# Kernel optimization log

Hardware: AMD Instinct MI355X
Metric: run time of the kernel (lower is better)

## Reference

```python
import jax, jax.numpy as jnp
import numpy as np

D_MODEL = 512
D_FF = 2048
N_EXPERTS = 8


def setup_inputs() -> dict:
    key = jax.random.key(0)
    ks = jax.random.split(key, 7)
    scale_in = 1.0 / np.sqrt(D_MODEL)
    scale_ff = 1.0 / np.sqrt(D_FF)
    x = jax.random.normal(ks[0], (4, 2048, D_MODEL), dtype=jnp.float32)
    w1 = jax.random.uniform(ks[1], (N_EXPERTS, D_MODEL, D_FF), jnp.float32, -scale_in, scale_in)
    b1 = jax.random.uniform(ks[2], (N_EXPERTS, D_FF), jnp.float32, -scale_in, scale_in)
    w2 = jax.random.uniform(ks[3], (N_EXPERTS, D_FF, D_MODEL), jnp.float32, -scale_ff, scale_ff)
    b2 = jax.random.uniform(ks[4], (N_EXPERTS, D_MODEL), jnp.float32, -scale_ff, scale_ff)
    wr = jax.random.uniform(ks[5], (D_MODEL, N_EXPERTS), jnp.float32, -scale_in, scale_in)
    br = jax.random.uniform(ks[6], (N_EXPERTS,), jnp.float32, -scale_in, scale_in)
    return {"x": x, "w1": w1, "b1": b1, "w2": w2, "b2": b2, "wr": wr, "br": br}


def reference(x, w1, b1, w2, b2, wr, br):
    # router softmax over experts: [b, t, e]
    route_weights = jax.nn.softmax(x @ wr + br, axis=-1)
    # all-experts FFN: h: [e, b, t, f]
    h = jax.nn.gelu(jnp.einsum('btd,edf->ebtf', x, w1) + b1[:, None, None, :],
                    approximate=False)
    # expert outputs weighted-summed: [b, t, d]
    expert_out = jnp.einsum('ebtf,efd->ebtd', h, w2) + b2[:, None, None, :]
    final_output = jnp.einsum('ebtd,bte->btd', expert_out, route_weights)
    return final_output, route_weights
```

## Files before the change

### kernel.cpp

```cpp
#include <hip/hip_runtime.h>
#include <math.h>

#define D_MODEL 512
#define D_FF    2048
#define N_EXP   8
#define N_TOK   8192
#define BM      64
#define BF      64

typedef _Float16 half8 __attribute__((ext_vector_type(8)));
typedef float    f32x4 __attribute__((ext_vector_type(4)));

__device__ __forceinline__ void gload_lds16(const void* g, void* lds) {
  __builtin_amdgcn_global_load_lds(
      (const __attribute__((address_space(1))) unsigned int*)g,
      (__attribute__((address_space(3))) unsigned int*)lds, 16, 0, 0);
}

__global__ void cvt_x_kernel(const float* __restrict__ x, _Float16* __restrict__ xb) {
  int i = blockIdx.x * blockDim.x + threadIdx.x;
  const float4* xp = (const float4*)x + (size_t)i * 2;
  float4 v0 = xp[0], v1 = xp[1];
  half8 o;
  o[0] = (_Float16)v0.x; o[1] = (_Float16)v0.y; o[2] = (_Float16)v0.z; o[3] = (_Float16)v0.w;
  o[4] = (_Float16)v1.x; o[5] = (_Float16)v1.y; o[6] = (_Float16)v1.z; o[7] = (_Float16)v1.w;
  ((half8*)xb)[i] = o;
}

__global__ void transpose_cvt_kernel(const float* __restrict__ in, _Float16* __restrict__ out,
                                     int R, int C) {
  __shared__ float t[32][33];
  int e = blockIdx.z, rb = blockIdx.y, cb = blockIdx.x;
  int tx = threadIdx.x & 31, ty = threadIdx.x >> 5;
  const float* src = in + ((size_t)e * R + rb * 32) * C + cb * 32;
#pragma unroll
  for (int i = 0; i < 32; i += 8) t[ty + i][tx] = src[(size_t)(ty + i) * C + tx];
  __syncthreads();
  _Float16* dst = out + ((size_t)e * C + cb * 32) * R + rb * 32;
#pragma unroll
  for (int i = 0; i < 32; i += 8) dst[(size_t)(ty + i) * R + tx] = (_Float16)t[tx][ty + i];
}

__global__ void router_kernel(const float* __restrict__ x, const float* __restrict__ wr,
                              const float* __restrict__ br, float* __restrict__ route) {
  int t = (blockIdx.x * blockDim.x + threadIdx.x) >> 6;
  int lane = threadIdx.x & 63;
  const float4* xp = (const float4*)(x + (size_t)t * D_MODEL) + lane * 2;
  float4 xv0 = xp[0], xv1 = xp[1];
  float xv[8] = {xv0.x, xv0.y, xv0.z, xv0.w, xv1.x, xv1.y, xv1.z, xv1.w};
  float acc[8] = {0, 0, 0, 0, 0, 0, 0, 0};
  int d0 = lane * 8;
#pragma unroll
  for (int i = 0; i < 8; ++i) {
    const float4* wp = (const float4*)(wr + (size_t)(d0 + i) * N_EXP);
    float4 w0 = wp[0], w1v = wp[1];
    acc[0] += xv[i] * w0.x;  acc[1] += xv[i] * w0.y;
    acc[2] += xv[i] * w0.z;  acc[3] += xv[i] * w0.w;
    acc[4] += xv[i] * w1v.x; acc[5] += xv[i] * w1v.y;
    acc[6] += xv[i] * w1v.z; acc[7] += xv[i] * w1v.w;
  }
#pragma unroll
  for (int off = 32; off > 0; off >>= 1)
#pragma unroll
    for (int e2 = 0; e2 < 8; ++e2) acc[e2] += __shfl_xor(acc[e2], off);
  float mx = -1e30f;
#pragma unroll
  for (int e2 = 0; e2 < 8; ++e2) { acc[e2] += br[e2]; mx = fmaxf(mx, acc[e2]); }
  float s = 0.f;
#pragma unroll
  for (int e2 = 0; e2 < 8; ++e2) { acc[e2] = expf(acc[e2] - mx); s += acc[e2]; }
  float inv = 1.f / s;
  if (lane < 8) route[(size_t)t * N_EXP + lane] = acc[lane] * inv;
}

__device__ __forceinline__ void stage_A_half(const _Float16* __restrict__ w1t, int e, int f0,
                                             int khalf, char* dst, int w, int l, int i0) {
#pragma unroll
  for (int i = i0; i < i0 + 2; ++i) {
    const int n  = i * 8 + w;
    const int f  = 2 * n + (l >> 5);
    const int sp = (l & 31) ^ (f & 31);
    gload_lds16(w1t + ((size_t)e * D_FF + f0 + f) * D_MODEL + khalf * 256 + sp * 8,
                dst + n * 1024);
  }
}
__device__ __forceinline__ void stage_B_half(const _Float16* __restrict__ w2t, int e, int f0,
                                             int dh, char* dst, int w, int l, int i0) {
#pragma unroll
  for (int i = i0; i < i0 + 2; ++i) {
    const int n  = i * 8 + w;
    const int d  = 8 * n + (l >> 3);
    const int sp = (l & 7) ^ (d & 7);
    gload_lds16(w2t + ((size_t)e * D_MODEL + dh * 256 + d) * D_FF + f0 + sp * 8,
                dst + n * 1024);
  }
}

__global__ __launch_bounds__(512, 2)
void moe_main_kernel(const _Float16* __restrict__ xb, const _Float16* __restrict__ w1t,
                     const _Float16* __restrict__ w2t, const float* __restrict__ b1,
                     const float* __restrict__ b2, const float* __restrict__ route,
                     float* __restrict__ out) {
  __shared__ __align__(16) unsigned char chA[2][32768];
  __shared__ __align__(16) unsigned char chB[2][32768];
  __shared__ __align__(16) unsigned char hs[BM * 128];
  __shared__ _Float16 b1_lds[4 * D_FF];
  __shared__ float routes_lds[4][BM];

  const int tid = threadIdx.x;
  const int l   = tid & 63;
  const int w   = tid >> 6;
  const int eb  = 4 * blockIdx.y;
  const int m0  = blockIdx.x * BM;

  const int mq  = w & 3;
  const int fh  = w >> 2;
  const int mh2 = w & 1;
  const int dq4 = w >> 1;

#pragma unroll
  for (int i = 0; i < 16; ++i) {
    int idx = i * 512 + tid;
    b1_lds[idx] = (_Float16)b1[(size_t)(eb + (idx >> 11)) * D_FF + (idx & 2047)];
  }
  if (tid < 4 * BM)
    routes_lds[tid >> 6][tid & 63] = route[(size_t)(m0 + (tid & 63)) * N_EXP + eb + (tid >> 6)];
  asm volatile("s_waitcnt lgkmcnt(0)" ::: "memory");

  half8 xfrag[16];
  {
    const _Float16* xrow = xb + (size_t)(m0 + 16 * mq + (l & 15)) * D_MODEL + (l >> 4) * 8;
#pragma unroll
    for (int ks = 0; ks < 16; ++ks)
      xfrag[ks] = *(const half8*)(xrow + ks * 32);
  }

  f32x4 acc[2][8];
#pragma unroll
  for (int a = 0; a < 2; ++a)
#pragma unroll
    for (int b = 0; b < 8; ++b) acc[a][b] = (f32x4){0.f, 0.f, 0.f, 0.f};

  stage_A_half(w1t, eb, 0, 0, (char*)chA[0], w, l, 0);
  stage_A_half(w1t, eb, 0, 0, (char*)chA[0], w, l, 2);
  stage_A_half(w1t, eb, 0, 1, (char*)chA[1], w, l, 0);
  stage_A_half(w1t, eb, 0, 1, (char*)chA[1], w, l, 2);
  stage_B_half(w2t, eb, 0, 0, (char*)chB[0], w, l, 0);
  stage_B_half(w2t, eb, 0, 0, (char*)chB[0], w, l, 2);
  asm volatile("s_waitcnt vmcnt(8)" ::: "memory");
  __builtin_amdgcn_s_barrier();

#pragma unroll 1
  for (int ei = 0; ei < 4; ++ei) {
    const int e = eb + ei;
#pragma unroll 1
    for (int fc = 0; fc < 32; ++fc) {
      const int f0 = fc * BF;
      int f0N = f0 + BF, eN = e;
      if (f0N == D_FF) { f0N = 0; eN = (ei < 3) ? e + 1 : eb; }

      float b1v[2];
#pragma unroll
      for (int j = 0; j < 2; ++j)
        b1v[j] = (float)b1_lds[ei * D_FF + f0 + 32 * fh + 16 * j + (l & 15)];

      f32x4 hacc[2];
      hacc[0] = (f32x4){0.f, 0.f, 0.f, 0.f};
      hacc[1] = (f32x4){0.f, 0.f, 0.f, 0.f};

#pragma unroll
      for (int kq = 0; kq < 4; ++kq) {
        const unsigned char* cA = chA[kq >> 1];
        const int q = kq & 1;
        half8 bfr[4][2];
#pragma unroll
        for (int t = 0; t < 4; ++t)
#pragma unroll
          for (int j = 0; j < 2; ++j) {
            const int f  = 32 * fh + 16 * j + (l & 15);
            const int g  = q * 16 + t * 4 + (l >> 4);
            const int sw = (g ^ f) & 31;
            bfr[t][j] = *(const half8*)(cA + f * 512 + sw * 16);
          }
        if      (kq == 0) stage_B_half(w2t, e,  f0,  1, (char*)chB[1], w, l, 0);
        else if (kq == 1) stage_B_half(w2t, e,  f0,  1, (char*)chB[1], w, l, 2);
        else if (kq == 2) stage_A_half(w1t, eN, f0N, 0, (char*)chA[0], w, l, 0);
        else              stage_A_half(w1t, eN, f0N, 0, (char*)chA[0], w, l, 2);
        if (kq & 1) asm volatile("s_waitcnt vmcnt(8)" ::: "memory");
        __builtin_amdgcn_s_barrier();
        asm volatile("s_waitcnt lgkmcnt(0)" ::: "memory");
        __builtin_amdgcn_s_setprio(1);
#pragma unroll
        for (int t = 0; t < 4; ++t) {
          hacc[0] = __builtin_amdgcn_mfma_f32_16x16x32_f16(xfrag[kq * 4 + t], bfr[t][0], hacc[0], 0, 0, 0);
          hacc[1] = __builtin_amdgcn_mfma_f32_16x16x32_f16(xfrag[kq * 4 + t], bfr[t][1], hacc[1], 0, 0, 0);
        }
        __builtin_amdgcn_s_setprio(0);
        if (kq == 3) {
#pragma unroll
          for (int j = 0; j < 2; ++j) {
#pragma unroll
            for (int r = 0; r < 4; ++r) {
              const int m      = 16 * mq + (l >> 4) * 4 + r;
              const int flocal = 32 * fh + 16 * j + (l & 15);
              float v  = hacc[j][r] + b1v[j];
              float u  = v * (1.5957691f + 0.0713548f * v * v);
              float E  = __expf(u);
              float gl = v * E / (E + 1.0f);
              gl *= routes_lds[ei][m];
              const int sh = (flocal >> 3) ^ ((m ^ (m >> 1)) & 7);
              *(_Float16*)(hs + m * 128 + sh * 16 + (flocal & 7) * 2) = (_Float16)gl;
            }
          }
          asm volatile("s_waitcnt lgkmcnt(0)" ::: "memory");
        }
        __builtin_amdgcn_s_barrier();
      }

      half8 a2c[2][2];
#pragma unroll
      for (int c = 0; c < 4; ++c) {
        const int h  = c >> 1;
        const int kh = c & 1;
        if (h == 0) {
#pragma unroll
          for (int mi2 = 0; mi2 < 2; ++mi2) {
            const int mr = 32 * mh2 + 16 * mi2 + (l & 15);
            const int sh = (kh * 4 + (l >> 4)) ^ ((mr ^ (mr >> 1)) & 7);
            a2c[kh][mi2] = *(const half8*)(hs + mr * 128 + sh * 16);
          }
        }
        half8 b2f[4];
#pragma unroll
        for (int jn = 0; jn < 4; ++jn) {
          const int row = dq4 * 64 + jn * 16 + (l & 15);
          const int sw  = (kh * 4 + (l >> 4)) ^ (row & 7);
          b2f[jn] = *(const half8*)(chB[h] + row * 128 + sw * 16);
        }
        if      (c == 0) stage_A_half(w1t, eN, f0N, 1, (char*)chA[1], w, l, 0);
        else if (c == 1) stage_A_half(w1t, eN, f0N, 1, (char*)chA[1], w, l, 2);
        else if (c == 2) stage_B_half(w2t, eN, f0N, 0, (char*)chB[0], w, l, 0);
        else             stage_B_half(w2t, eN, f0N, 0, (char*)chB[0], w, l, 2);
        if (c & 1) asm volatile("s_waitcnt vmcnt(8)" ::: "memory");
        __builtin_amdgcn_s_barrier();
        asm volatile("s_waitcnt lgkmcnt(0)" ::: "memory");
        __builtin_amdgcn_s_setprio(1);
#pragma unroll
        for (int jn = 0; jn < 4; ++jn) {
          acc[0][h * 4 + jn] = __builtin_amdgcn_mfma_f32_16x16x32_f16(a2c[kh][0], b2f[jn], acc[0][h * 4 + jn], 0, 0, 0);
          acc[1][h * 4 + jn] = __builtin_amdgcn_mfma_f32_16x16x32_f16(a2c[kh][1], b2f[jn], acc[1][h * 4 + jn], 0, 0, 0);
        }
        __builtin_amdgcn_s_setprio(0);
        __builtin_amdgcn_s_barrier();
      }
    }
  }

  asm volatile("s_waitcnt vmcnt(0)" ::: "memory");

#pragma unroll
  for (int h = 0; h < 2; ++h)
#pragma unroll
    for (int jn = 0; jn < 4; ++jn) {
      const int dcol = h * 256 + dq4 * 64 + jn * 16 + (l & 15);
      float b2v[4];
#pragma unroll
      for (int ei = 0; ei < 4; ++ei) b2v[ei] = b2[(size_t)(eb + ei) * D_MODEL + dcol];
#pragma unroll
      for (int mi2 = 0; mi2 < 2; ++mi2)
#pragma unroll
        for (int r = 0; r < 4; ++r) {
          const int m = 32 * mh2 + 16 * mi2 + (l >> 4) * 4 + r;
          float add = 0.f;
#pragma unroll
          for (int ei = 0; ei < 4; ++ei) add += routes_lds[ei][m] * b2v[ei];
          unsafeAtomicAdd(out + (size_t)(m0 + m) * D_MODEL + dcol, acc[mi2][h * 4 + jn][r] + add);
        }
    }
}

extern "C" void kernel_launch(void* const* d_in, const int* in_sizes, int n_in,
                              void* d_out, int out_size, void* d_ws, size_t ws_size,
                              hipStream_t stream) {
  (void)in_sizes; (void)n_in; (void)out_size; (void)ws_size;
  const float* x  = (const float*)d_in[0];
  const float* w1 = (const float*)d_in[1];
  const float* b1 = (const float*)d_in[2];
  const float* w2 = (const float*)d_in[3];
  const float* b2 = (const float*)d_in[4];
  const float* wr = (const float*)d_in[5];
  const float* br = (const float*)d_in[6];
  float* out   = (float*)d_out;
  float* route = out + (size_t)N_TOK * D_MODEL;

  char* ws = (char*)d_ws;
  _Float16* xb  = (_Float16*)ws;
  _Float16* w1t = (_Float16*)(ws + (size_t)N_TOK * D_MODEL * 2);
  _Float16* w2t = (_Float16*)(ws + (size_t)N_TOK * D_MODEL * 2
                                 + (size_t)N_EXP * D_FF * D_MODEL * 2);

  hipMemsetAsync(out, 0, (size_t)N_TOK * D_MODEL * sizeof(float), stream);
  cvt_x_kernel<<<(N_TOK * D_MODEL / 8) / 256, 256, 0, stream>>>(x, xb);
  transpose_cvt_kernel<<<dim3(D_FF / 32, D_MODEL / 32, N_EXP), 256, 0, stream>>>(w1, w1t, D_MODEL, D_FF);
  transpose_cvt_kernel<<<dim3(D_MODEL / 32, D_FF / 32, N_EXP), 256, 0, stream>>>(w2, w2t, D_FF, D_MODEL);
  router_kernel<<<N_TOK / 4, 256, 0, stream>>>(x, wr, br, route);
  moe_main_kernel<<<dim3(N_TOK / BM, 2), 512, 0, stream>>>(xb, w1t, w2t, b1, b2, route, out);
}
```

Baseline: 457.9 us.

## Split GEMM1 K-dimension across wave groups and cut per-step barriers

Changes the first GEMM's work split: instead of each wave owning a 16-row M slice over the full K, waves now own 32x32 output tiles over half of K. The two partial sums are reduced through the shared-memory h buffer before GELU. Prefetch staging and barriers are reorganized so far fewer s_barrier calls run per F chunk. The goal is to lower synchronization overhead and halve the per-wave x fragment registers. The cost is an extra LDS round trip for the reduction, and the hand-tuned vmcnt waits carry a correctness risk if they are wrong.

Result: slower. 615.2 us (+34.3%).

```diff
diff --git a/kernel.cpp b/kernel.cpp
--- a/kernel.cpp
+++ b/kernel.cpp
@@ -113,8 +113,9 @@
   const int eb  = 4 * blockIdx.y;
   const int m0  = blockIdx.x * BM;
 
-  const int mq  = w & 3;
-  const int fh  = w >> 2;
+  const int mh1 = w & 1;
+  const int fh1 = (w >> 1) & 1;
+  const int khg = w >> 2;
   const int mh2 = w & 1;
   const int dq4 = w >> 1;
 
@@ -127,12 +128,14 @@
     routes_lds[tid >> 6][tid & 63] = route[(size_t)(m0 + (tid & 63)) * N_EXP + eb + (tid >> 6)];
   asm volatile("s_waitcnt lgkmcnt(0)" ::: "memory");
 
-  half8 xfrag[16];
-  {
-    const _Float16* xrow = xb + (size_t)(m0 + 16 * mq + (l & 15)) * D_MODEL + (l >> 4) * 8;
-#pragma unroll
-    for (int ks = 0; ks < 16; ++ks)
-      xfrag[ks] = *(const half8*)(xrow + ks * 32);
+  half8 xfrag[2][8];
+#pragma unroll
+  for (int mi = 0; mi < 2; ++mi) {
+    const _Float16* xrow = xb + (size_t)(m0 + 32 * mh1 + 16 * mi + (l & 15)) * D_MODEL
+                              + khg * 256 + (l >> 4) * 8;
+#pragma unroll
+    for (int ks = 0; ks < 8; ++ks)
+      xfrag[mi][ks] = *(const half8*)(xrow + ks * 32);
   }
 
   f32x4 acc[2][8];
@@ -147,7 +150,6 @@
   stage_A_half(w1t, eb, 0, 1, (char*)chA[1], w, l, 2);
   stage_B_half(w2t, eb, 0, 0, (char*)chB[0], w, l, 0);
   stage_B_half(w2t, eb, 0, 0, (char*)chB[0], w, l, 2);
-  asm volatile("s_waitcnt vmcnt(8)" ::: "memory");
   __builtin_amdgcn_s_barrier();
 
 #pragma unroll 1
@@ -159,69 +161,102 @@
       int f0N = f0 + BF, eN = e;
       if (f0N == D_FF) { f0N = 0; eN = (ei < 3) ? e + 1 : eb; }
 
-      float b1v[2];
-#pragma unroll
-      for (int j = 0; j < 2; ++j)
-        b1v[j] = (float)b1_lds[ei * D_FF + f0 + 32 * fh + 16 * j + (l & 15)];
-
-      f32x4 hacc[2];
-      hacc[0] = (f32x4){0.f, 0.f, 0.f, 0.f};
-      hacc[1] = (f32x4){0.f, 0.f, 0.f, 0.f};
-
-#pragma unroll
-      for (int kq = 0; kq < 4; ++kq) {
-        const unsigned char* cA = chA[kq >> 1];
-        const int q = kq & 1;
-        half8 bfr[4][2];
-#pragma unroll
-        for (int t = 0; t < 4; ++t)
+      f32x4 hacc[2][2];
+#pragma unroll
+      for (int mi = 0; mi < 2; ++mi)
+#pragma unroll
+        for (int j = 0; j < 2; ++j) hacc[mi][j] = (f32x4){0.f, 0.f, 0.f, 0.f};
+
+#pragma unroll
+      for (int p = 0; p < 4; ++p) {
+        if (p == 0) {
+          stage_B_half(w2t, e, f0, 1, (char*)chB[1], w, l, 0);
+          asm volatile("s_waitcnt vmcnt(6)" ::: "memory");
+          __builtin_amdgcn_s_barrier();
+        } else if (p == 1) {
+          stage_B_half(w2t, e, f0, 1, (char*)chB[1], w, l, 2);
+        }
+        half8 bfr[2][2];
+#pragma unroll
+        for (int ks2 = 0; ks2 < 2; ++ks2)
 #pragma unroll
           for (int j = 0; j < 2; ++j) {
-            const int f  = 32 * fh + 16 * j + (l & 15);
-            const int g  = q * 16 + t * 4 + (l >> 4);
+            const int f  = 32 * fh1 + 16 * j + (l & 15);
+            const int g  = (p * 2 + ks2) * 4 + (l >> 4);
             const int sw = (g ^ f) & 31;
-            bfr[t][j] = *(const half8*)(cA + f * 512 + sw * 16);
+            bfr[ks2][j] = *(const half8*)(chA[khg] + f * 512 + sw * 16);
           }
-        if      (kq == 0) stage_B_half(w2t, e,  f0,  1, (char*)chB[1], w, l, 0);
-        else if (kq == 1) stage_B_half(w2t, e,  f0,  1, (char*)chB[1], w, l, 2);
-        else if (kq == 2) stage_A_half(w1t, eN, f0N, 0, (char*)chA[0], w, l, 0);
-        else              stage_A_half(w1t, eN, f0N, 0, (char*)chA[0], w, l, 2);
-        if (kq & 1) asm volatile("s_waitcnt vmcnt(8)" ::: "memory");
-        __builtin_amdgcn_s_barrier();
         asm volatile("s_waitcnt lgkmcnt(0)" ::: "memory");
         __builtin_amdgcn_s_setprio(1);
 #pragma unroll
-        for (int t = 0; t < 4; ++t) {
-          hacc[0] = __builtin_amdgcn_mfma_f32_16x16x32_f16(xfrag[kq * 4 + t], bfr[t][0], hacc[0], 0, 0, 0);
-          hacc[1] = __builtin_amdgcn_mfma_f32_16x16x32_f16(xfrag[kq * 4 + t], bfr[t][1], hacc[1], 0, 0, 0);
-        }
+        for (int ks2 = 0; ks2 < 2; ++ks2)
+#pragma unroll
+          for (int j = 0; j < 2; ++j) {
+            hacc[0][j] = __builtin_amdgcn_mfma_f32_16x16x32_f16(xfrag[0][p * 2 + ks2], bfr[ks2][j], hacc[0][j], 0, 0, 0);
+            hacc[1][j] = __builtin_amdgcn_mfma_f32_16x16x32_f16(xfrag[1][p * 2 + ks2], bfr[ks2][j], hacc[1][j], 0, 0, 0);
+          }
         __builtin_amdgcn_s_setprio(0);
-        if (kq == 3) {
-#pragma unroll
-          for (int j = 0; j < 2; ++j) {
+      }
+
+      if (khg == 0) {
+#pragma unroll
+        for (int mi = 0; mi < 2; ++mi)
+#pragma unroll
+          for (int j = 0; j < 2; ++j)
 #pragma unroll
             for (int r = 0; r < 4; ++r) {
-              const int m      = 16 * mq + (l >> 4) * 4 + r;
-              const int flocal = 32 * fh + 16 * j + (l & 15);
-              float v  = hacc[j][r] + b1v[j];
+              const int m  = 32 * mh1 + 16 * mi + (l >> 4) * 4 + r;
+              const int fl = 32 * fh1 + 16 * j + (l & 15);
+              const int sh = (fl >> 3) ^ ((m ^ (m >> 1)) & 7);
+              *(_Float16*)(hs + m * 128 + sh * 16 + (fl & 7) * 2) = (_Float16)hacc[mi][j][r];
+            }
+        asm volatile("s_waitcnt lgkmcnt(0)" ::: "memory");
+      }
+      __builtin_amdgcn_s_barrier();
+      if (khg == 1) {
+        float b1v[2];
+#pragma unroll
+        for (int j = 0; j < 2; ++j)
+          b1v[j] = (float)b1_lds[ei * D_FF + f0 + 32 * fh1 + 16 * j + (l & 15)];
+#pragma unroll
+        for (int mi = 0; mi < 2; ++mi)
+#pragma unroll
+          for (int j = 0; j < 2; ++j)
+#pragma unroll
+            for (int r = 0; r < 4; ++r) {
+              const int m  = 32 * mh1 + 16 * mi + (l >> 4) * 4 + r;
+              const int fl = 32 * fh1 + 16 * j + (l & 15);
+              const int sh = (fl >> 3) ^ ((m ^ (m >> 1)) & 7);
+              _Float16* ptr = (_Float16*)(hs + m * 128 + sh * 16 + (fl & 7) * 2);
+              float v  = (float)*ptr + hacc[mi][j][r] + b1v[j];
               float u  = v * (1.5957691f + 0.0713548f * v * v);
               float E  = __expf(u);
               float gl = v * E / (E + 1.0f);
               gl *= routes_lds[ei][m];
-              const int sh = (flocal >> 3) ^ ((m ^ (m >> 1)) & 7);
-              *(_Float16*)(hs + m * 128 + sh * 16 + (flocal & 7) * 2) = (_Float16)gl;
+              *ptr = (_Float16)gl;
             }
-          }
-          asm volatile("s_waitcnt lgkmcnt(0)" ::: "memory");
-        }
-        __builtin_amdgcn_s_barrier();
+        asm volatile("s_waitcnt lgkmcnt(0)" ::: "memory");
       }
+      asm volatile("s_waitcnt vmcnt(4)" ::: "memory");
+      __builtin_amdgcn_s_barrier();
 
       half8 a2c[2][2];
 #pragma unroll
       for (int c = 0; c < 4; ++c) {
         const int h  = c >> 1;
         const int kh = c & 1;
+        if (c == 0) {
+          stage_A_half(w1t, eN, f0N, 0, (char*)chA[0], w, l, 0);
+          stage_A_half(w1t, eN, f0N, 0, (char*)chA[0], w, l, 2);
+        } else if (c == 1) {
+          stage_A_half(w1t, eN, f0N, 1, (char*)chA[1], w, l, 0);
+          stage_A_half(w1t, eN, f0N, 1, (char*)chA[1], w, l, 2);
+          asm volatile("s_waitcnt vmcnt(8)" ::: "memory");
+          __builtin_amdgcn_s_barrier();
+        } else if (c == 2) {
+          stage_B_half(w2t, eN, f0N, 0, (char*)chB[0], w, l, 0);
+          stage_B_half(w2t, eN, f0N, 0, (char*)chB[0], w, l, 2);
+        }
         if (h == 0) {
 #pragma unroll
           for (int mi2 = 0; mi2 < 2; ++mi2) {
@@ -237,12 +272,6 @@
           const int sw  = (kh * 4 + (l >> 4)) ^ (row & 7);
           b2f[jn] = *(const half8*)(chB[h] + row * 128 + sw * 16);
         }
-        if      (c == 0) stage_A_half(w1t, eN, f0N, 1, (char*)chA[1], w, l, 0);
-        else if (c == 1) stage_A_half(w1t, eN, f0N, 1, (char*)chA[1], w, l, 2);
-        else if (c == 2) stage_B_half(w2t, eN, f0N, 0, (char*)chB[0], w, l, 0);
-        else             stage_B_half(w2t, eN, f0N, 0, (char*)chB[0], w, l, 2);
-        if (c & 1) asm volatile("s_waitcnt vmcnt(8)" ::: "memory");
-        __builtin_amdgcn_s_barrier();
         asm volatile("s_waitcnt lgkmcnt(0)" ::: "memory");
         __builtin_amdgcn_s_setprio(1);
 #pragma unroll
@@ -251,7 +280,6 @@
           acc[1][h * 4 + jn] = __builtin_amdgcn_mfma_f32_16x16x32_f16(a2c[kh][1], b2f[jn], acc[1][h * 4 + jn], 0, 0, 0);
         }
         __builtin_amdgcn_s_setprio(0);
-        __builtin_amdgcn_s_barrier();
       }
     }
   }
```
